# Kernel optimization log

Measured on AMD Instinct MI355X. Metric: run time of the kernel, lower is better.

The kernel has to match this reference:

```python
import jax, jax.numpy as jnp
import numpy as np

B = 32          # batch_size
M = 1024        # mesh_num (nodes per sub-graph)
D_IN = 128      # sub_node_feature_input_dim
D_OUT = 128     # sub_node_feature_output_dim
E_DIM = 64      # embedding dim per node


def setup_inputs() -> dict:
    key = jax.random.key(0)
    k1, k2, k3, k4 = jax.random.split(key, 4)
    return {
        "node_feature_group": jax.random.normal(k1, (B * M, D_IN), dtype=jnp.float32),
        "embedding_group": jax.random.normal(k2, (B * M, E_DIM), dtype=jnp.float32),
        "W1": jax.random.normal(k3, (D_OUT, D_IN), dtype=jnp.float32) * (1.0 / np.sqrt(D_IN)),
        "W2": jax.random.normal(k4, (D_OUT, D_OUT), dtype=jnp.float32) * (1.0 / np.sqrt(D_OUT)),
    }


def reference(node_feature_group, embedding_group, W1, W2):
    # The torch module builds a (B*M)x(B*M) block-diagonal adjacency via
    # torch.block_diag; off-block entries are exactly zero, and row sums /
    # D^-1/2 A D^-1/2 normalization act per block, so we compute per-graph.
    E = embedding_group.reshape(B, M, E_DIM)
    adj = jnp.maximum(jnp.einsum('bme,bne->bmn', E, E), 0.0)  # clamp(E E^T, 0)
    adj = adj + jnp.eye(M, dtype=adj.dtype)                   # A = adj + I
    d = adj.sum(-1)                                           # [B, M]
    dinv = d ** -0.5                                          # symmetric=True
    dad = dinv[:, :, None] * adj * dinv[:, None, :]           # D^-1/2 A D^-1/2

    X = node_feature_group.reshape(B, M, D_IN)
    y = jax.nn.relu(jnp.einsum('bmn,bnd->bmd', dad, X) @ W1.T)   # gcn1
    y = jax.nn.relu(jnp.einsum('bmn,bnd->bmd', dad, y) @ W2.T)   # gcn2
    # Dropout is identity in eval mode.
    return y.reshape(B * M, D_OUT)
```

## Files before the change

kernel.cpp:

```cpp
#include <hip/hip_runtime.h>
#include <stdint.h>

#define B_  32
#define M_  1024
#define DF  128
#define ED  64

typedef __attribute__((ext_vector_type(8))) short short8;
typedef __attribute__((ext_vector_type(4))) float floatx4;

__device__ inline unsigned short f2bf(float f) {
    union { float f; unsigned u; } v; v.f = f;
    unsigned r = v.u + 0x7fffu + ((v.u >> 16) & 1u);
    return (unsigned short)(r >> 16);
}

__device__ inline void load_lds16(const void* g, void* l) {
    __builtin_amdgcn_global_load_lds(
        (const __attribute__((address_space(1))) unsigned int*)g,
        (__attribute__((address_space(3))) unsigned int*)l, 16, 0, 0);
}

__global__ __launch_bounds__(256) void cast_kernel(
    const float* __restrict__ E, const float* __restrict__ W1,
    const float* __restrict__ W2, unsigned short* __restrict__ Ebf,
    unsigned short* __restrict__ W1bf, unsigned short* __restrict__ W2bf) {
    const int NE = B_ * M_ * ED;
    const int NW = DF * DF;
    int idx = (blockIdx.x * 256 + threadIdx.x) * 4;
    const float* src; unsigned short* dst; int off;
    if (idx < NE)            { src = E;  dst = Ebf;  off = idx; }
    else if (idx < NE + NW)  { src = W1; dst = W1bf; off = idx - NE; }
    else                     { src = W2; dst = W2bf; off = idx - NE - NW; }
    float4 v = *(const float4*)(src + off);
    ushort4 o;
    o.x = f2bf(v.x); o.y = f2bf(v.y); o.z = f2bf(v.z); o.w = f2bf(v.w);
    *(ushort4*)(dst + off) = o;
}

__global__ __launch_bounds__(256) void build_s_kernel(
    const unsigned short* __restrict__ Ebf, const float* __restrict__ X,
    unsigned short* __restrict__ S, float* __restrict__ dinv,
    unsigned short* __restrict__ Xt) {
    int mt2 = blockIdx.x, b = blockIdx.y;
    int t = threadIdx.x;
    int w = t >> 6, lane = t & 63, quad = lane >> 4, lc = lane & 15;
    __shared__ unsigned short sEn[128][72];
    __shared__ unsigned short sOut[128 * 72];
    __shared__ float sDinv[64];
    const unsigned short* Eb = Ebf + (size_t)b * M_ * ED;
    unsigned short* Sg = S + ((size_t)b << 20);
    int m0 = mt2 * 64;
    int base_m = m0 + w * 16;

    short8 afr[2];
    for (int ks = 0; ks < 2; ++ks)
        afr[ks] = *(const short8*)(Eb + (size_t)(base_m + lc) * ED + ks * 32 + quad * 8);
    floatx4 rsum = (floatx4){0.f, 0.f, 0.f, 0.f};

    for (int nc = 0; nc < 8; ++nc) {
        __syncthreads();
        for (int it = 0; it < 4; ++it) {
            int c = t + 256 * it;
            int row = c >> 3, off = (c & 7) * 8;
            *(short8*)(&sEn[row][off]) =
                *(const short8*)(Eb + (size_t)(nc * 128 + row) * ED + off);
        }
        __syncthreads();
        for (int nt = 0; nt < 8; ++nt) {
            short8 b0 = *(const short8*)(&sEn[nt * 16 + lc][quad * 8]);
            short8 b1 = *(const short8*)(&sEn[nt * 16 + lc][32 + quad * 8]);
            floatx4 s = (floatx4){0.f, 0.f, 0.f, 0.f};
            s = __builtin_amdgcn_mfma_f32_16x16x32_bf16(afr[0], b0, s, 0, 0, 0);
            s = __builtin_amdgcn_mfma_f32_16x16x32_bf16(afr[1], b1, s, 0, 0, 0);
            int n = nc * 128 + nt * 16 + lc;
            for (int r = 0; r < 4; ++r) {
                int m = base_m + quad * 4 + r;
                float v = fmaxf(s[r], 0.f);
                if (m == n) v += 1.0f;
                rsum[r] += v;
                sOut[(w * 16 + quad * 4 + r) * 136 + nt * 16 + lc] = f2bf(v);
            }
        }
        __syncthreads();
        for (int it = 0; it < 4; ++it) {
            int c = t + 256 * it;
            int lrow = c >> 4, noff = (c & 15) * 8;
            *(short8*)(Sg + (size_t)(m0 + lrow) * M_ + nc * 128 + noff) =
                *(const short8*)(&sOut[lrow * 136 + noff]);
        }
    }
    for (int r = 0; r < 4; ++r) {
        float v = rsum[r];
        v += __shfl_xor(v, 1, 16);
        v += __shfl_xor(v, 2, 16);
        v += __shfl_xor(v, 4, 16);
        v += __shfl_xor(v, 8, 16);
        if (lc == 0) {
            float dv = rsqrtf(v);
            int lrow = w * 16 + quad * 4 + r;
            dinv[b * M_ + m0 + lrow] = dv;
            sDinv[lrow] = dv;
        }
    }
    __syncthreads();
    unsigned short* sXT = sOut;
    {
        int nloc = t >> 5;
        int d4 = (t & 31) * 4;
        for (int pass = 0; pass < 8; ++pass) {
            int n = pass * 8 + nloc;
            float sc = sDinv[n];
            float4 v = *(const float4*)(X + (size_t)(b * M_ + m0 + n) * DF + d4);
            sXT[(d4 + 0) * 72 + n] = f2bf(v.x * sc);
            sXT[(d4 + 1) * 72 + n] = f2bf(v.y * sc);
            sXT[(d4 + 2) * 72 + n] = f2bf(v.z * sc);
            sXT[(d4 + 3) * 72 + n] = f2bf(v.w * sc);
        }
    }
    __syncthreads();
    for (int it = 0; it < 4; ++it) {
        int c = t + 256 * it;
        int d = c >> 3, off = (c & 7) * 8;
        *(short8*)(Xt + (size_t)(b * DF + d) * M_ + m0 + off) =
            *(const short8*)(&sXT[d * 72 + off]);
    }
}

template <int MODE>
__global__ __launch_bounds__(256) void gemm_kernel(
    const unsigned short* __restrict__ S,
    const unsigned short* __restrict__ Pt,
    const unsigned short* __restrict__ Wbf,
    const float* __restrict__ dinv,
    unsigned short* __restrict__ OutT,
    float* __restrict__ OutF) {
    int bx = blockIdx.x, b = blockIdx.y;
    int m0 = bx * 64;
    int t = threadIdx.x;
    int w = t >> 6, lane = t & 63, quad = lane >> 4, lc = lane & 15;
    int wr = w & 1, wc = w >> 1;

    __shared__ __align__(16) unsigned short lds[26112];
    unsigned short* sA = lds;
    unsigned short* sB = lds + 4096;
    unsigned short* sY = lds;
    unsigned short* sW = lds + 8704;

    const unsigned short* Sg = S + ((size_t)b << 20);
    const unsigned short* Pb = Pt + (size_t)b * DF * M_;

    floatx4 acc[2][4];
    for (int i = 0; i < 2; ++i)
        for (int j = 0; j < 4; ++j) acc[i][j] = (floatx4){0.f, 0.f, 0.f, 0.f};

    for (int nc = 0; nc < 16; ++nc) {
        __syncthreads();
        for (int r = 0; r < 2; ++r) {
            int c = r * 256 + w * 64 + lane;
            const void* gp = Sg + (size_t)(m0 + (c >> 3)) * M_ + nc * 64 + (c & 7) * 8;
            load_lds16(gp, (char*)sA + c * 16);
        }
        for (int r = 0; r < 4; ++r) {
            int c = r * 256 + w * 64 + lane;
            const void* gp = Pb + (size_t)(c >> 3) * M_ + nc * 64 + (c & 7) * 8;
            load_lds16(gp, (char*)sB + c * 16);
        }
        __syncthreads();
        for (int ks = 0; ks < 2; ++ks) {
            short8 afr[2], bfr[4];
            for (int i = 0; i < 2; ++i)
                afr[i] = *(const short8*)(&sA[(wr * 32 + i * 16 + lc) * 64 + ks * 32 + quad * 8]);
            for (int j = 0; j < 4; ++j)
                bfr[j] = *(const short8*)(&sB[(wc * 64 + j * 16 + lc) * 64 + ks * 32 + quad * 8]);
            for (int i = 0; i < 2; ++i)
                for (int j = 0; j < 4; ++j)
                    acc[i][j] = __builtin_amdgcn_mfma_f32_16x16x32_bf16(afr[i], bfr[j], acc[i][j], 0, 0, 0);
        }
    }

    float dv[2][4];
    for (int i = 0; i < 2; ++i)
        for (int r = 0; r < 4; ++r)
            dv[i][r] = dinv[b * M_ + m0 + wr * 32 + i * 16 + quad * 4 + r];
    __syncthreads();
    for (int i = 0; i < 2; ++i)
        for (int j = 0; j < 4; ++j) {
            int mrow = wr * 32 + i * 16 + quad * 4;
            int col = wc * 64 + j * 16 + lc;
            for (int r = 0; r < 4; ++r)
                sY[(mrow + r) * 136 + col] = f2bf(acc[i][j][r] * dv[i][r]);
        }
    for (int it = 0; it < 8; ++it) {
        int c = t + 256 * it;
        int row = c >> 4, off = (c & 15) * 8;
        *(short8*)(&sW[row * 136 + off]) = *(const short8*)(Wbf + row * DF + off);
    }
    __syncthreads();
    floatx4 accH[2][4];
    for (int i = 0; i < 2; ++i)
        for (int j = 0; j < 4; ++j) accH[i][j] = (floatx4){0.f, 0.f, 0.f, 0.f};
    for (int ks = 0; ks < 4; ++ks) {
        short8 afr[2], bfr[4];
        for (int i = 0; i < 2; ++i)
            afr[i] = *(const short8*)(&sY[(wr * 32 + i * 16 + lc) * 136 + ks * 32 + quad * 8]);
        for (int j = 0; j < 4; ++j)
            bfr[j] = *(const short8*)(&sW[(wc * 64 + j * 16 + lc) * 136 + ks * 32 + quad * 8]);
        for (int i = 0; i < 2; ++i)
            for (int j = 0; j < 4; ++j)
                accH[i][j] = __builtin_amdgcn_mfma_f32_16x16x32_bf16(afr[i], bfr[j], accH[i][j], 0, 0, 0);
    }
    if (MODE == 2) {
        float* Ob = OutF + ((size_t)b * M_ + m0) * DF;
        for (int i = 0; i < 2; ++i)
            for (int j = 0; j < 4; ++j) {
                int mrow = wr * 32 + i * 16 + quad * 4;
                int col = wc * 64 + j * 16 + lc;
                for (int r = 0; r < 4; ++r)
                    Ob[(size_t)(mrow + r) * DF + col] = fmaxf(accH[i][j][r], 0.f);
            }
    } else {
        __syncthreads();
        unsigned short* sT = sW;
        for (int i = 0; i < 2; ++i)
            for (int j = 0; j < 4; ++j) {
                int mrow = wr * 32 + i * 16 + quad * 4;
                int col = wc * 64 + j * 16 + lc;
                for (int r = 0; r < 4; ++r)
                    sT[col * 72 + mrow + r] = f2bf(fmaxf(accH[i][j][r], 0.f) * dv[i][r]);
            }
        __syncthreads();
        for (int it = 0; it < 4; ++it) {
            int c = t + 256 * it;
            int o = c >> 3, moff = (c & 7) * 8;
            *(short8*)(OutT + (size_t)(b * DF + o) * M_ + m0 + moff) =
                *(const short8*)(&sT[o * 72 + moff]);
        }
    }
}

extern "C" void kernel_launch(void* const* d_in, const int* in_sizes, int n_in,
                              void* d_out, int out_size, void* d_ws, size_t ws_size,
                              hipStream_t stream) {
    (void)in_sizes; (void)n_in; (void)out_size; (void)ws_size;
    const float* X  = (const float*)d_in[0];
    const float* E  = (const float*)d_in[1];
    const float* W1 = (const float*)d_in[2];
    const float* W2 = (const float*)d_in[3];
    float* out = (float*)d_out;

    char* ws = (char*)d_ws;
    unsigned short* Ebf  = (unsigned short*)(ws);
    unsigned short* W1bf = (unsigned short*)(ws + 4194304);
    unsigned short* W2bf = (unsigned short*)(ws + 4227072);
    float*          dinv = (float*)(ws + 4259840);
    unsigned short* Xt   = (unsigned short*)(ws + 4390912);
    unsigned short* Ht   = (unsigned short*)(ws + 12779520);
    unsigned short* Smat = (unsigned short*)(ws + 21168128);

    cast_kernel<<<2080, 256, 0, stream>>>(E, W1, W2, Ebf, W1bf, W2bf);
    build_s_kernel<<<dim3(16, 32), 256, 0, stream>>>(Ebf, X, Smat, dinv, Xt);
    gemm_kernel<1><<<dim3(16, 32), 256, 0, stream>>>(Smat, Xt, W1bf, dinv, Ht, nullptr);
    gemm_kernel<2><<<dim3(16, 32), 256, 0, stream>>>(Smat, Ht, W2bf, dinv, nullptr, out);
}
```

Before: 155.4 us.

## Load MFMA operand fragments directly from global memory instead of LDS staging

```diff
diff --git a/kernel.cpp b/kernel.cpp
--- a/kernel.cpp
+++ b/kernel.cpp
@@ -13,12 +13,6 @@
     union { float f; unsigned u; } v; v.f = f;
     unsigned r = v.u + 0x7fffu + ((v.u >> 16) & 1u);
     return (unsigned short)(r >> 16);
-}
-
-__device__ inline void load_lds16(const void* g, void* l) {
-    __builtin_amdgcn_global_load_lds(
-        (const __attribute__((address_space(1))) unsigned int*)g,
-        (__attribute__((address_space(3))) unsigned int*)l, 16, 0, 0);
 }
 
 __global__ __launch_bounds__(256) void cast_kernel(
@@ -45,7 +39,6 @@
     int mt2 = blockIdx.x, b = blockIdx.y;
     int t = threadIdx.x;
     int w = t >> 6, lane = t & 63, quad = lane >> 4, lc = lane & 15;
-    __shared__ unsigned short sEn[128][72];
     __shared__ unsigned short sOut[128 * 72];
     __shared__ float sDinv[64];
     const unsigned short* Eb = Ebf + (size_t)b * M_ * ED;
@@ -60,16 +53,10 @@
 
     for (int nc = 0; nc < 8; ++nc) {
         __syncthreads();
-        for (int it = 0; it < 4; ++it) {
-            int c = t + 256 * it;
-            int row = c >> 3, off = (c & 7) * 8;
-            *(short8*)(&sEn[row][off]) =
-                *(const short8*)(Eb + (size_t)(nc * 128 + row) * ED + off);
-        }
-        __syncthreads();
         for (int nt = 0; nt < 8; ++nt) {
-            short8 b0 = *(const short8*)(&sEn[nt * 16 + lc][quad * 8]);
-            short8 b1 = *(const short8*)(&sEn[nt * 16 + lc][32 + quad * 8]);
+            int nrow = nc * 128 + nt * 16 + lc;
+            short8 b0 = *(const short8*)(Eb + (size_t)nrow * ED + quad * 8);
+            short8 b1 = *(const short8*)(Eb + (size_t)nrow * ED + 32 + quad * 8);
             floatx4 s = (floatx4){0.f, 0.f, 0.f, 0.f};
             s = __builtin_amdgcn_mfma_f32_16x16x32_bf16(afr[0], b0, s, 0, 0, 0);
             s = __builtin_amdgcn_mfma_f32_16x16x32_bf16(afr[1], b1, s, 0, 0, 0);
@@ -142,48 +129,38 @@
     int wr = w & 1, wc = w >> 1;
 
     __shared__ __align__(16) unsigned short lds[26112];
-    unsigned short* sA = lds;
-    unsigned short* sB = lds + 4096;
     unsigned short* sY = lds;
     unsigned short* sW = lds + 8704;
 
-    const unsigned short* Sg = S + ((size_t)b << 20);
-    const unsigned short* Pb = Pt + (size_t)b * DF * M_;
+    const unsigned short* Sa = S + ((size_t)b << 20) +
+                               (size_t)(m0 + wr * 32 + lc) * M_ + quad * 8;
+    const unsigned short* Pb = Pt + (size_t)b * DF * M_ +
+                               (size_t)(wc * 64 + lc) * M_ + quad * 8;
 
     floatx4 acc[2][4];
     for (int i = 0; i < 2; ++i)
         for (int j = 0; j < 4; ++j) acc[i][j] = (floatx4){0.f, 0.f, 0.f, 0.f};
 
     for (int nc = 0; nc < 16; ++nc) {
-        __syncthreads();
-        for (int r = 0; r < 2; ++r) {
-            int c = r * 256 + w * 64 + lane;
-            const void* gp = Sg + (size_t)(m0 + (c >> 3)) * M_ + nc * 64 + (c & 7) * 8;
-            load_lds16(gp, (char*)sA + c * 16);
-        }
-        for (int r = 0; r < 4; ++r) {
-            int c = r * 256 + w * 64 + lane;
-            const void* gp = Pb + (size_t)(c >> 3) * M_ + nc * 64 + (c & 7) * 8;
-            load_lds16(gp, (char*)sB + c * 16);
-        }
-        __syncthreads();
+        short8 afr[2][2], bfr[2][4];
         for (int ks = 0; ks < 2; ++ks) {
-            short8 afr[2], bfr[4];
+            int ko = nc * 64 + ks * 32;
             for (int i = 0; i < 2; ++i)
-                afr[i] = *(const short8*)(&sA[(wr * 32 + i * 16 + lc) * 64 + ks * 32 + quad * 8]);
+                afr[ks][i] = *(const short8*)(Sa + (size_t)(i * 16) * M_ + ko);
             for (int j = 0; j < 4; ++j)
-                bfr[j] = *(const short8*)(&sB[(wc * 64 + j * 16 + lc) * 64 + ks * 32 + quad * 8]);
+                bfr[ks][j] = *(const short8*)(Pb + (size_t)(j * 16) * M_ + ko);
+        }
+        for (int ks = 0; ks < 2; ++ks)
             for (int i = 0; i < 2; ++i)
                 for (int j = 0; j < 4; ++j)
-                    acc[i][j] = __builtin_amdgcn_mfma_f32_16x16x32_bf16(afr[i], bfr[j], acc[i][j], 0, 0, 0);
-        }
+                    acc[i][j] = __builtin_amdgcn_mfma_f32_16x16x32_bf16(
+                        afr[ks][i], bfr[ks][j], acc[i][j], 0, 0, 0);
     }
 
     float dv[2][4];
     for (int i = 0; i < 2; ++i)
         for (int r = 0; r < 4; ++r)
             dv[i][r] = dinv[b * M_ + m0 + wr * 32 + i * 16 + quad * 4 + r];
-    __syncthreads();
     for (int i = 0; i < 2; ++i)
         for (int j = 0; j < 4; ++j) {
             int mrow = wr * 32 + i * 16 + quad * 4;
```

After: 216.4 us. 1.39x slower.
